# Performance work log

Measured on AMD Instinct MI355X. Metric: run time of the kernel, lower is better.

The kernel has to match this reference:

```python
import jax, jax.numpy as jnp
import numpy as np

NUM_GRAPHS = 64
EPS = 1e-5


def setup_inputs() -> dict:
    key = jax.random.key(0)
    ks = jax.random.split(key, 10)
    N, E, D, H = 100000, 600000, 128, 128
    inputs = jax.random.normal(ks[0], (N, D), dtype=jnp.float32)
    edge_index = jax.random.randint(ks[1], (2, E), 0, N, dtype=jnp.int64)
    batch = jnp.sort(jax.random.randint(ks[2], (N,), 0, NUM_GRAPHS, dtype=jnp.int64))
    edge_weight = jax.random.uniform(ks[3], (E,), dtype=jnp.float32)
    # learned params: GCNConv linear (glorot) + bias, GraphNorm affine params
    W = jax.random.normal(ks[4], (D, H), dtype=jnp.float32) * (1.0 / np.sqrt(D))
    b = jnp.zeros((H,), dtype=jnp.float32)
    gn_weight = jnp.ones((H,), dtype=jnp.float32)
    gn_bias = jnp.zeros((H,), dtype=jnp.float32)
    gn_alpha = jnp.ones((H,), dtype=jnp.float32)  # GraphNorm mean_scale
    return {"inputs": inputs, "edge_index": edge_index, "batch": batch,
            "edge_weight": edge_weight, "W": W, "b": b,
            "gn_weight": gn_weight, "gn_bias": gn_bias, "gn_alpha": gn_alpha}


def reference(inputs, edge_index, batch, edge_weight, W, b, gn_weight, gn_bias, gn_alpha):
    N = inputs.shape[0]
    # ---- GCNConv with symmetric normalization and added self-loops ----
    loop = jnp.arange(N, dtype=edge_index.dtype)
    row = jnp.concatenate([edge_index[0], loop])  # source nodes
    col = jnp.concatenate([edge_index[1], loop])  # target nodes
    w = jnp.concatenate([edge_weight, jnp.ones((N,), dtype=edge_weight.dtype)])
    deg = jax.ops.segment_sum(w, col, num_segments=N)  # in-degree (weighted)
    dis = jnp.where(deg > 0, jax.lax.rsqrt(deg), 0.0)
    norm = dis[row] * w * dis[col]  # [E+N]
    x = inputs @ W  # [N, H]
    msg = x[row] * norm[:, None]  # gather + scale
    out = jax.ops.segment_sum(msg, col, num_segments=N) + b  # scatter-add
    # ---- GraphNorm: per-graph mean/var with learnable mean scale alpha ----
    cnt = jax.ops.segment_sum(jnp.ones((N,), dtype=out.dtype), batch,
                              num_segments=NUM_GRAPHS)
    cnt = jnp.maximum(cnt, 1.0)[:, None]  # [G,1]
    mean = jax.ops.segment_sum(out, batch, num_segments=NUM_GRAPHS) / cnt
    sub = out - gn_alpha * mean[batch]
    var = jax.ops.segment_sum(sub * sub, batch, num_segments=NUM_GRAPHS) / cnt
    h = sub * jax.lax.rsqrt(var[batch] + EPS) * gn_weight + gn_bias
    # ---- relu (add_residue=False) + global max pool ----
    h = jax.nn.relu(h)
    flat = jax.ops.segment_max(h, batch, num_segments=NUM_GRAPHS)
    return h, flat
```

## Files before the change

### kernel.cpp

```cpp
#include <hip/hip_runtime.h>
#include <math.h>

typedef float f4 __attribute__((ext_vector_type(4)));
typedef float f2 __attribute__((ext_vector_type(2)));

#define NUM_G 64
#define CH 16
#define EPSV 1e-5f

__device__ inline f4 f4_max(f4 a, f4 b) {
  f4 r;
#pragma unroll
  for (int i = 0; i < 4; ++i) r[i] = fmaxf(a[i], b[i]);
  return r;
}

__global__ void k_init(const int* __restrict__ batch, float* __restrict__ deg,
                       int* __restrict__ ecnt, int* __restrict__ gstart, int N) {
  int n = blockIdx.x * blockDim.x + threadIdx.x;
  if (n >= N) return;
  deg[n] = 1.0f;
  ecnt[n] = 0;
  int bn = batch[n];
  int bp = (n == 0) ? -1 : batch[n - 1];
  for (int g = bp + 1; g <= bn; ++g) gstart[g] = n;
  if (n == N - 1) {
    for (int g = bn + 1; g <= NUM_G; ++g) gstart[g] = N;
  }
}

__global__ void k_deg(const int* __restrict__ col, const float* __restrict__ ew,
                      float* __restrict__ deg, int* __restrict__ ecnt, int E) {
  int e = blockIdx.x * blockDim.x + threadIdx.x;
  if (e >= E) return;
  int c = col[e];
  atomicAdd(&deg[c], ew[e]);
  atomicAdd(&ecnt[c], 1);
}

__global__ __launch_bounds__(256) void k_scanA(const int* __restrict__ ecnt,
                                               int* __restrict__ bsum, int N) {
  __shared__ int sb[256];
  int n = blockIdx.x * 256 + threadIdx.x;
  sb[threadIdx.x] = (n < N) ? ecnt[n] : 0;
  __syncthreads();
  for (int o = 128; o >= 1; o >>= 1) {
    if (threadIdx.x < o) sb[threadIdx.x] += sb[threadIdx.x + o];
    __syncthreads();
  }
  if (threadIdx.x == 0) bsum[blockIdx.x] = sb[0];
}

__global__ __launch_bounds__(1024) void k_scanB(int* __restrict__ bsum,
                                                int* __restrict__ off, int NB, int N) {
  __shared__ int sb[1024];
  int t = threadIdx.x;
  int sc = (NB + 1023) >> 10;
  int s = t * sc, e = min(s + sc, NB);
  int local = 0;
  for (int i = s; i < e; ++i) local += bsum[i];
  sb[t] = local;
  __syncthreads();
  for (int o = 1; o < 1024; o <<= 1) {
    int v = sb[t];
    int a = (t >= o) ? sb[t - o] : 0;
    __syncthreads();
    sb[t] = v + a;
    __syncthreads();
  }
  int running = sb[t] - local;
  for (int i = s; i < e; ++i) {
    int v = bsum[i];
    bsum[i] = running;
    running += v;
  }
  if (t == 0) off[N] = sb[1023];
}

__global__ __launch_bounds__(256) void k_scanC(const int* __restrict__ ecnt,
                                               const int* __restrict__ bsum,
                                               const float* __restrict__ deg,
                                               int* __restrict__ off, int* __restrict__ cursor,
                                               float* __restrict__ dis, int N) {
  __shared__ int sb[256];
  int n = blockIdx.x * 256 + threadIdx.x;
  int v = (n < N) ? ecnt[n] : 0;
  sb[threadIdx.x] = v;
  __syncthreads();
  for (int o = 1; o < 256; o <<= 1) {
    int x = sb[threadIdx.x];
    int a = (threadIdx.x >= o) ? sb[threadIdx.x - o] : 0;
    __syncthreads();
    sb[threadIdx.x] = x + a;
    __syncthreads();
  }
  if (n < N) {
    int ex = bsum[blockIdx.x] + sb[threadIdx.x] - v;
    off[n] = ex;
    cursor[n] = ex;
    float d = deg[n];
    dis[n] = (d > 0.f) ? (1.0f / sqrtf(d)) : 0.f;
  }
}

__global__ __launch_bounds__(512) void k_gemm(const float* __restrict__ in,
                                              const float* __restrict__ Wg,
                                              float* __restrict__ x, int N, int ntiles) {
  __shared__ float Wl[128 * 128];
  f4* Wl4 = (f4*)Wl;
  const f4* Wg4 = (const f4*)Wg;
  for (int i = threadIdx.x; i < 4096; i += 512) Wl4[i] = Wg4[i];
  __syncthreads();
  int lane = threadIdx.x & 31;
  int rg = threadIdx.x >> 5;
  for (int tile = blockIdx.x; tile < ntiles; tile += gridDim.x) {
    int r0 = tile * 64 + rg * 4;
    bool ok0 = r0 + 0 < N, ok1 = r0 + 1 < N, ok2 = r0 + 2 < N, ok3 = r0 + 3 < N;
    const f4* a0 = (const f4*)(in + (size_t)(ok0 ? r0 + 0 : 0) * 128);
    const f4* a1 = (const f4*)(in + (size_t)(ok1 ? r0 + 1 : 0) * 128);
    const f4* a2 = (const f4*)(in + (size_t)(ok2 ? r0 + 2 : 0) * 128);
    const f4* a3 = (const f4*)(in + (size_t)(ok3 ? r0 + 3 : 0) * 128);
    f4 acc0 = (f4)0.f, acc1 = (f4)0.f, acc2 = (f4)0.f, acc3 = (f4)0.f;
#pragma unroll 4
    for (int k4 = 0; k4 < 32; ++k4) {
      f4 a0v = a0[k4], a1v = a1[k4], a2v = a2[k4], a3v = a3[k4];
#pragma unroll
      for (int kk = 0; kk < 4; ++kk) {
        f4 wv = Wl4[(k4 * 4 + kk) * 32 + lane];
        acc0 += a0v[kk] * wv;
        acc1 += a1v[kk] * wv;
        acc2 += a2v[kk] * wv;
        acc3 += a3v[kk] * wv;
      }
    }
    if (ok0) ((f4*)(x + (size_t)(r0 + 0) * 128))[lane] = acc0;
    if (ok1) ((f4*)(x + (size_t)(r0 + 1) * 128))[lane] = acc1;
    if (ok2) ((f4*)(x + (size_t)(r0 + 2) * 128))[lane] = acc2;
    if (ok3) ((f4*)(x + (size_t)(r0 + 3) * 128))[lane] = acc3;
  }
}

__global__ void k_scatter(const int* __restrict__ row, const int* __restrict__ col,
                          const float* __restrict__ ew, const float* __restrict__ dis,
                          int* __restrict__ cursor, int* __restrict__ srow,
                          float* __restrict__ snorm, int E) {
  int e = blockIdx.x * blockDim.x + threadIdx.x;
  if (e >= E) return;
  int r = row[e], c = col[e];
  float nm = dis[r] * ew[e] * dis[c];
  int p = atomicAdd(&cursor[c], 1);
  srow[p] = r;
  snorm[p] = nm;
}

__global__ __launch_bounds__(256) void k_accum(const float* __restrict__ x,
                                               const float* __restrict__ dis,
                                               const int* __restrict__ off,
                                               const int* __restrict__ srow,
                                               const float* __restrict__ snorm,
                                               const float* __restrict__ bias,
                                               float* __restrict__ out, int N) {
  int lane = threadIdx.x & 63;
  int sub = threadIdx.x >> 6;
  int n = blockIdx.x * 4 + sub;
  if (n >= N) return;
  const f2* x2 = (const f2*)x;
  float dn = dis[n];
  f2 acc0 = x2[(size_t)n * 64 + lane] * (dn * dn);
  f2 acc1 = (f2)0.f, acc2 = (f2)0.f, acc3 = (f2)0.f;
  int s = off[n], e = off[n + 1];
  int i = s;
  for (; i + 4 <= e; i += 4) {
    int r0 = srow[i], r1 = srow[i + 1], r2 = srow[i + 2], r3 = srow[i + 3];
    float n0 = snorm[i], n1 = snorm[i + 1], n2 = snorm[i + 2], n3 = snorm[i + 3];
    acc0 += x2[(size_t)r0 * 64 + lane] * n0;
    acc1 += x2[(size_t)r1 * 64 + lane] * n1;
    acc2 += x2[(size_t)r2 * 64 + lane] * n2;
    acc3 += x2[(size_t)r3 * 64 + lane] * n3;
  }
  for (; i < e; ++i) acc0 += x2[(size_t)srow[i] * 64 + lane] * snorm[i];
  acc0 += (acc1 + acc2) + (acc3 + ((const f2*)bias)[lane]);
  ((f2*)out)[(size_t)n * 64 + lane] = acc0;
}

__global__ __launch_bounds__(256) void k_stats(const float* __restrict__ out,
                                               const int* __restrict__ gstart,
                                               float* __restrict__ Ssum,
                                               float* __restrict__ Ssq) {
  int g = blockIdx.x / CH, c = blockIdx.x % CH;
  int s = gstart[g], e = gstart[g + 1];
  int len = e - s;
  int csz = (len + CH - 1) / CH;
  int r0 = s + c * csz, r1 = min(r0 + csz, e);
  int lane = threadIdx.x & 31, rg = threadIdx.x >> 5;
  const f4* out4 = (const f4*)out;
  f4 acc = (f4)0.f, accq = (f4)0.f;
  for (int r = r0 + rg; r < r1; r += 8) {
    f4 v = out4[(size_t)r * 32 + lane];
    acc += v;
    accq += v * v;
  }
  __shared__ f4 red[256], redq[256];
  red[threadIdx.x] = acc;
  redq[threadIdx.x] = accq;
  __syncthreads();
  for (int st = 4; st >= 1; st >>= 1) {
    if (rg < st) {
      red[threadIdx.x] += red[threadIdx.x + st * 32];
      redq[threadIdx.x] += redq[threadIdx.x + st * 32];
    }
    __syncthreads();
  }
  if (rg == 0) {
    ((f4*)Ssum)[(size_t)(g * CH + c) * 32 + lane] = red[threadIdx.x];
    ((f4*)Ssq)[(size_t)(g * CH + c) * 32 + lane] = redq[threadIdx.x];
  }
}

__global__ __launch_bounds__(256) void k_final(float* __restrict__ out,
                                               const int* __restrict__ gstart,
                                               const float* __restrict__ Ssum,
                                               const float* __restrict__ Ssq,
                                               const float* __restrict__ alpha,
                                               const float* __restrict__ gw,
                                               const float* __restrict__ gb,
                                               float* __restrict__ Pmax) {
  int g = blockIdx.x / CH, c = blockIdx.x % CH;
  int s = gstart[g], e = gstart[g + 1];
  int len = e - s;
  float inv_cnt = 1.0f / (float)((len < 1) ? 1 : len);
  __shared__ f4 aml[32], istdl[32];
  int lane = threadIdx.x & 31, rg = threadIdx.x >> 5;
  if (threadIdx.x < 32) {
    f4 m = (f4)0.f, q = (f4)0.f;
    for (int cc = 0; cc < CH; ++cc) {
      m += ((const f4*)Ssum)[(size_t)(g * CH + cc) * 32 + threadIdx.x];
      q += ((const f4*)Ssq)[(size_t)(g * CH + cc) * 32 + threadIdx.x];
    }
    m *= inv_cnt;
    q *= inv_cnt;
    f4 al = ((const f4*)alpha)[threadIdx.x];
    f4 am = al * m;
    f4 var = q - 2.0f * am * m + am * am;
    f4 is;
#pragma unroll
    for (int i = 0; i < 4; ++i) is[i] = 1.0f / sqrtf(var[i] + EPSV);
    aml[threadIdx.x] = am;
    istdl[threadIdx.x] = is;
  }
  __syncthreads();
  int csz = (len + CH - 1) / CH;
  int r0 = s + c * csz, r1 = min(r0 + csz, e);
  f4 am = aml[lane];
  f4 is = istdl[lane];
  f4 w4 = ((const f4*)gw)[lane];
  f4 b4 = ((const f4*)gb)[lane];
  f4* out4 = (f4*)out;
  f4 mx = (f4)0.f;
  for (int r = r0 + rg; r < r1; r += 8) {
    f4 o = out4[(size_t)r * 32 + lane];
    f4 h = (o - am) * is * w4 + b4;
    h = f4_max(h, (f4)0.f);
    out4[(size_t)r * 32 + lane] = h;
    mx = f4_max(mx, h);
  }
  __shared__ f4 red[256];
  red[threadIdx.x] = mx;
  __syncthreads();
  for (int st = 4; st >= 1; st >>= 1) {
    if (rg < st) red[threadIdx.x] = f4_max(red[threadIdx.x], red[threadIdx.x + st * 32]);
    __syncthreads();
  }
  if (rg == 0) ((f4*)Pmax)[(size_t)(g * CH + c) * 32 + lane] = red[threadIdx.x];
}

__global__ void k_flat(const float* __restrict__ Pmax, float* __restrict__ flat) {
  int g = blockIdx.x;
  int f = threadIdx.x;
  float m = 0.f;
  for (int c = 0; c < CH; ++c) m = fmaxf(m, Pmax[((size_t)g * CH + c) * 128 + f]);
  flat[g * 128 + f] = m;
}

extern "C" void kernel_launch(void* const* d_in, const int* in_sizes, int n_in,
                              void* d_out, int out_size, void* d_ws, size_t ws_size,
                              hipStream_t stream) {
  const float* inputs = (const float*)d_in[0];
  const int* eidx = (const int*)d_in[1];
  const int* batch = (const int*)d_in[2];
  const float* ew = (const float*)d_in[3];
  const float* Wg = (const float*)d_in[4];
  const float* bias = (const float*)d_in[5];
  const float* gw = (const float*)d_in[6];
  const float* gb = (const float*)d_in[7];
  const float* galpha = (const float*)d_in[8];

  int N = in_sizes[0] / 128;
  int E = in_sizes[1] / 2;
  const int* erow = eidx;
  const int* ecol = eidx + E;

  char* w = (char*)d_ws;
  auto alloc = [&](size_t bytes) {
    char* p = w;
    w += (bytes + 255) & ~(size_t)255;
    return p;
  };
  float* x = (float*)alloc((size_t)N * 128 * 4);
  float* deg = (float*)alloc((size_t)N * 4);
  float* dis = (float*)alloc((size_t)N * 4);
  int* ecnt = (int*)alloc((size_t)N * 4);
  int* off = (int*)alloc((size_t)(N + 1) * 4);
  int* cursor = (int*)alloc((size_t)N * 4);
  int* srow = (int*)alloc((size_t)E * 4);
  float* snorm = (float*)alloc((size_t)E * 4);
  int* gstart = (int*)alloc((size_t)(NUM_G + 1) * 4);
  float* Ssum = (float*)alloc((size_t)NUM_G * CH * 128 * 4);
  float* Ssq = (float*)alloc((size_t)NUM_G * CH * 128 * 4);
  float* Pmax = (float*)alloc((size_t)NUM_G * CH * 128 * 4);
  int NB = (N + 255) / 256;
  int* bsum = (int*)alloc((size_t)NB * 4);

  float* outh = (float*)d_out;
  float* flat = outh + (size_t)N * 128;

  k_init<<<(N + 255) / 256, 256, 0, stream>>>(batch, deg, ecnt, gstart, N);
  k_deg<<<(E + 255) / 256, 256, 0, stream>>>(ecol, ew, deg, ecnt, E);
  k_scanA<<<NB, 256, 0, stream>>>(ecnt, bsum, N);
  k_scanB<<<1, 1024, 0, stream>>>(bsum, off, NB, N);
  k_scanC<<<NB, 256, 0, stream>>>(ecnt, bsum, deg, off, cursor, dis, N);
  int ntiles = (N + 63) / 64;
  k_gemm<<<ntiles, 512, 0, stream>>>(inputs, Wg, x, N, ntiles);
  k_scatter<<<(E + 255) / 256, 256, 0, stream>>>(erow, ecol, ew, dis, cursor, srow, snorm, E);
  k_accum<<<(N + 3) / 4, 256, 0, stream>>>(x, dis, off, srow, snorm, bias, outh, N);
  k_stats<<<NUM_G * CH, 256, 0, stream>>>(outh, gstart, Ssum, Ssq);
  k_final<<<NUM_G * CH, 256, 0, stream>>>(outh, gstart, Ssum, Ssq, galpha, gw, gb, Pmax);
  k_flat<<<NUM_G, 128, 0, stream>>>(Pmax, flat);
}
```

Measured before the change: 367.0 us.

## Tile GEMM over K with shared-memory staging of input rows and W chunks

The GEMM kernel no longer copies the whole 64KB W matrix into LDS per block. It now loops over four K-chunks of 32, staging a 64x32 input tile and a 32x128 slice of W in shared memory each iteration. Input rows are loaded with coalesced vector reads instead of per-thread strided global reads. This cuts LDS use from 64KB to about 24KB, which should raise occupancy, at the cost of extra barriers and reloading W per block.

```diff
diff --git a/kernel.cpp b/kernel.cpp
--- a/kernel.cpp
+++ b/kernel.cpp
@@ -105,39 +105,48 @@
 
 __global__ __launch_bounds__(512) void k_gemm(const float* __restrict__ in,
                                               const float* __restrict__ Wg,
-                                              float* __restrict__ x, int N, int ntiles) {
-  __shared__ float Wl[128 * 128];
-  f4* Wl4 = (f4*)Wl;
-  const f4* Wg4 = (const f4*)Wg;
-  for (int i = threadIdx.x; i < 4096; i += 512) Wl4[i] = Wg4[i];
-  __syncthreads();
-  int lane = threadIdx.x & 31;
-  int rg = threadIdx.x >> 5;
-  for (int tile = blockIdx.x; tile < ntiles; tile += gridDim.x) {
-    int r0 = tile * 64 + rg * 4;
-    bool ok0 = r0 + 0 < N, ok1 = r0 + 1 < N, ok2 = r0 + 2 < N, ok3 = r0 + 3 < N;
-    const f4* a0 = (const f4*)(in + (size_t)(ok0 ? r0 + 0 : 0) * 128);
-    const f4* a1 = (const f4*)(in + (size_t)(ok1 ? r0 + 1 : 0) * 128);
-    const f4* a2 = (const f4*)(in + (size_t)(ok2 ? r0 + 2 : 0) * 128);
-    const f4* a3 = (const f4*)(in + (size_t)(ok3 ? r0 + 3 : 0) * 128);
-    f4 acc0 = (f4)0.f, acc1 = (f4)0.f, acc2 = (f4)0.f, acc3 = (f4)0.f;
-#pragma unroll 4
-    for (int k4 = 0; k4 < 32; ++k4) {
-      f4 a0v = a0[k4], a1v = a1[k4], a2v = a2[k4], a3v = a3[k4];
+                                              float* __restrict__ x, int N) {
+  __shared__ float As[64][32];
+  __shared__ float Ws[32][128];
+  int tid = threadIdx.x;
+  int lane = tid & 31;
+  int rg = tid >> 5;
+  int brow = blockIdx.x * 64;
+  int ar = tid >> 3;
+  int aseg = (tid & 7) * 4;
+  const f4* wsrc0 = (const f4*)Wg;
+  f4 acc0 = (f4)0.f, acc1 = (f4)0.f, acc2 = (f4)0.f, acc3 = (f4)0.f;
+  for (int kc = 0; kc < 4; ++kc) {
+    int gr = brow + ar;
+    f4 av = (f4)0.f;
+    if (gr < N) av = *(const f4*)(in + (size_t)gr * 128 + kc * 32 + aseg);
+    *(f4*)&As[ar][aseg] = av;
+    const f4* wsrc = wsrc0 + (size_t)kc * 32 * 32;
+    ((f4*)Ws)[tid] = wsrc[tid];
+    ((f4*)Ws)[tid + 512] = wsrc[tid + 512];
+    __syncthreads();
+#pragma unroll
+    for (int k4 = 0; k4 < 8; ++k4) {
+      f4 a0 = *(const f4*)&As[rg * 4 + 0][k4 * 4];
+      f4 a1 = *(const f4*)&As[rg * 4 + 1][k4 * 4];
+      f4 a2 = *(const f4*)&As[rg * 4 + 2][k4 * 4];
+      f4 a3 = *(const f4*)&As[rg * 4 + 3][k4 * 4];
 #pragma unroll
       for (int kk = 0; kk < 4; ++kk) {
-        f4 wv = Wl4[(k4 * 4 + kk) * 32 + lane];
-        acc0 += a0v[kk] * wv;
-        acc1 += a1v[kk] * wv;
-        acc2 += a2v[kk] * wv;
-        acc3 += a3v[kk] * wv;
+        f4 wv = *(const f4*)&Ws[k4 * 4 + kk][lane * 4];
+        acc0 += a0[kk] * wv;
+        acc1 += a1[kk] * wv;
+        acc2 += a2[kk] * wv;
+        acc3 += a3[kk] * wv;
       }
     }
-    if (ok0) ((f4*)(x + (size_t)(r0 + 0) * 128))[lane] = acc0;
-    if (ok1) ((f4*)(x + (size_t)(r0 + 1) * 128))[lane] = acc1;
-    if (ok2) ((f4*)(x + (size_t)(r0 + 2) * 128))[lane] = acc2;
-    if (ok3) ((f4*)(x + (size_t)(r0 + 3) * 128))[lane] = acc3;
-  }
+    __syncthreads();
+  }
+  int r0 = brow + rg * 4;
+  if (r0 + 0 < N) ((f4*)(x + (size_t)(r0 + 0) * 128))[lane] = acc0;
+  if (r0 + 1 < N) ((f4*)(x + (size_t)(r0 + 1) * 128))[lane] = acc1;
+  if (r0 + 2 < N) ((f4*)(x + (size_t)(r0 + 2) * 128))[lane] = acc2;
+  if (r0 + 3 < N) ((f4*)(x + (size_t)(r0 + 3) * 128))[lane] = acc3;
 }
 
 __global__ void k_scatter(const int* __restrict__ row, const int* __restrict__ col,
@@ -329,8 +338,7 @@
   k_scanA<<<NB, 256, 0, stream>>>(ecnt, bsum, N);
   k_scanB<<<1, 1024, 0, stream>>>(bsum, off, NB, N);
   k_scanC<<<NB, 256, 0, stream>>>(ecnt, bsum, deg, off, cursor, dis, N);
-  int ntiles = (N + 63) / 64;
-  k_gemm<<<ntiles, 512, 0, stream>>>(inputs, Wg, x, N, ntiles);
+  k_gemm<<<(N + 63) / 64, 512, 0, stream>>>(inputs, Wg, x, N);
   k_scatter<<<(E + 255) / 256, 256, 0, stream>>>(erow, ecol, ew, dis, cursor, srow, snorm, E);
   k_accum<<<(N + 3) / 4, 256, 0, stream>>>(x, dis, off, srow, snorm, bias, outh, N);
   k_stats<<<NUM_G * CH, 256, 0, stream>>>(outh, gstart, Ssum, Ssq);
```

After: 339.4 us. 7.5% less time.
